# Optimization experiments

Measured on AMD Instinct MI355X. Metric: run time of the kernel, lower is better.

Reference implementation:

```python
import jax, jax.numpy as jnp
import numpy as np

N_CLASS = 32000
EMB = 512
HID = 1024
BATCH = 64
SEQ = 256


def setup_inputs() -> dict:
    key = jax.random.key(0)
    ks = jax.random.split(key, 24)
    X = jax.random.randint(ks[0], (BATCH, SEQ), 0, N_CLASS)
    C_emb = jax.random.normal(ks[1], (N_CLASS, EMB), dtype=jnp.float32) * 0.02
    d0 = HID + EMB   # layer-0 gate input dim (cat(h, x))
    d1 = HID + HID   # layer-1 gate input dim (cat(h, h_below))
    def w(k, din):
        return jax.random.normal(k, (din, HID), dtype=jnp.float32) * (1.0 / np.sqrt(din))
    inp = {
        'X': X, 'C_emb': C_emb,
        'W_i0': w(ks[2], d0), 'b_i0': jnp.ones((HID,), jnp.float32),
        'W_c0': w(ks[3], d0), 'b_c0': jnp.ones((HID,), jnp.float32),
        'W_f0': w(ks[4], d0), 'b_f0': jnp.ones((HID,), jnp.float32),
        'W_o0': w(ks[5], d0), 'b_o0': jnp.ones((HID,), jnp.float32),
        'W_i1': w(ks[6], d1), 'b_i1': jnp.ones((HID,), jnp.float32),
        'W_c1': w(ks[7], d1), 'b_c1': jnp.ones((HID,), jnp.float32),
        'W_f1': w(ks[8], d1), 'b_f1': jnp.ones((HID,), jnp.float32),
        'W_o1': w(ks[9], d1), 'b_o1': jnp.ones((HID,), jnp.float32),
        'W_out': jax.random.normal(ks[10], (HID, N_CLASS), jnp.float32) * (1.0 / np.sqrt(HID)),
        'b_out': jnp.ones((N_CLASS,), jnp.float32),
    }
    return inp


def _lstm_lm(X, C_emb, layers, W_out, b_out):
    B = X.shape[0]
    xs = jnp.transpose(C_emb[X], (1, 0, 2))  # (S, B, E)
    h0 = tuple(jnp.zeros((B, HID), xs.dtype) for _ in layers)
    c0 = tuple(jnp.zeros((B, HID), xs.dtype) for _ in layers)

    def step(carry, x_t):
        hs, cs = carry
        inp = x_t
        new_h, new_c = [], []
        for l, (Wi, bi, Wc, bc, Wf, bf, Wo, bo) in enumerate(layers):
            m = jnp.concatenate([hs[l], inp], axis=1)  # cat(h_state, input_below)
            i = jax.nn.sigmoid(m @ Wi + bi)
            g = jnp.tanh(m @ Wc + bc)
            f = jax.nn.sigmoid(m @ Wf + bf)
            c = f * cs[l] + i * g
            o = jax.nn.sigmoid(m @ Wo + bo)
            h = o * jnp.tanh(c)
            new_h.append(h)
            new_c.append(c)
            inp = h
        return (tuple(new_h), tuple(new_c)), None

    (hs, _), _ = jax.lax.scan(step, (h0, c0), xs)
    return hs[-1] @ W_out + b_out  # (B, n_class): logits from last timestep, top layer


def reference(X, C_emb, W_i0, b_i0, W_c0, b_c0, W_f0, b_f0, W_o0, b_o0,
              W_i1, b_i1, W_c1, b_c1, W_f1, b_f1, W_o1, b_o1, W_out, b_out):
    layers = [
        (W_i0, b_i0, W_c0, b_c0, W_f0, b_f0, W_o0, b_o0),
        (W_i1, b_i1, W_c1, b_c1, W_f1, b_f1, W_o1, b_o1),
    ]
    return _lstm_lm(X, C_emb, layers, W_out, b_out)
```

## Files before the change

### kernel.cpp

```cpp
#include <hip/hip_runtime.h>
#include <cstdint>
#include <cstddef>

#define NCLS 32000
#define EMBD 512
#define HIDD 1024
#define BATCH 64
#define SEQL 256
#define NWG 256
#define K0 1536
#define K1 2048
#define K0P (K0 + 2)
#define K1P (K1 + 2)
#define BH (BATCH * HIDD)
#define HBYTES (BH * 2)


typedef __attribute__((ext_vector_type(8))) short short8;
typedef __attribute__((ext_vector_type(4))) float float4v;
typedef unsigned long long ull;

#define WS_CTR   0
#define WS_H0G   2048
#define WS_H1G   (WS_H0G + 2*HBYTES)
#define WS_XEMB  (WS_H1G + 2*HBYTES)

#define SMEM_BYTES ((16*K0P + 16*K1P)*2 + (8192 + 32 + 512 + 8)*4)

__device__ __forceinline__ unsigned short f2bf(float f) {
  union { float f; uint32_t u; } x; x.f = f;
  uint32_t r = x.u + 0x7FFFu + ((x.u >> 16) & 1u);
  return (unsigned short)(r >> 16);
}

__device__ __forceinline__ float sigm(float x) {
  return 1.0f / (1.0f + __expf(-x));
}

__device__ __forceinline__ void gbar(unsigned* bar, unsigned* gen, unsigned* dead,
                                     unsigned target) {
  __syncthreads();
  if (threadIdx.x == 0) {
    unsigned prev = __hip_atomic_fetch_add(bar, 1u, __ATOMIC_RELAXED, __HIP_MEMORY_SCOPE_AGENT);
    if (prev == target * NWG - 1u) {
      __hip_atomic_store(gen, target, __ATOMIC_RELAXED, __HIP_MEMORY_SCOPE_AGENT);
    } else {
      unsigned spin = 0;
      while (__hip_atomic_load(gen, __ATOMIC_RELAXED, __HIP_MEMORY_SCOPE_AGENT) < target) {
        if (__hip_atomic_load(dead, __ATOMIC_RELAXED, __HIP_MEMORY_SCOPE_AGENT) != 0u) break;
        if (++spin > 2000000u) {
          __hip_atomic_store(dead, 1u, __ATOMIC_RELAXED, __HIP_MEMORY_SCOPE_AGENT);
          break;
        }
        __builtin_amdgcn_s_sleep(1);
      }
    }
  }
  __syncthreads();
}

__device__ __forceinline__ void hbar(unsigned* ctr, unsigned xcc, unsigned nloc,
                                     unsigned nxcd, unsigned tgt) {
  __syncthreads();
  if (threadIdx.x == 0) {
    unsigned* xctr = ctr + 64 + 16 * xcc;
    unsigned* xgen = ctr + 192 + 16 * xcc;
    unsigned* dead = ctr + 17;
    unsigned a = __hip_atomic_fetch_add(xctr, 1u, __ATOMIC_RELAXED, __HIP_MEMORY_SCOPE_AGENT);
    if (a == tgt * nloc - 1u) {
      asm volatile("buffer_inv sc1\n\ts_waitcnt vmcnt(0)" ::: "memory");
      unsigned g = __hip_atomic_fetch_add(ctr, 1u, __ATOMIC_RELAXED, __HIP_MEMORY_SCOPE_AGENT);
      if (g == tgt * nxcd - 1u) {
        __hip_atomic_store(ctr + 16, tgt, __ATOMIC_RELAXED, __HIP_MEMORY_SCOPE_AGENT);
      } else {
        unsigned spin = 0;
        while (__hip_atomic_load(ctr + 16, __ATOMIC_RELAXED, __HIP_MEMORY_SCOPE_AGENT) < tgt) {
          if ((++spin & 63u) == 0u) {
            if (__hip_atomic_load(dead, __ATOMIC_RELAXED, __HIP_MEMORY_SCOPE_AGENT) != 0u) break;
            if (spin > 4000000u) {
              __hip_atomic_store(dead, 1u, __ATOMIC_RELAXED, __HIP_MEMORY_SCOPE_AGENT);
              break;
            }
          }
        }
      }
      __hip_atomic_store(xgen, tgt, __ATOMIC_RELAXED, __HIP_MEMORY_SCOPE_AGENT);
    } else {
      unsigned spin = 0;
      while (__hip_atomic_load(xgen, __ATOMIC_RELAXED, __HIP_MEMORY_SCOPE_AGENT) < tgt) {
        if ((++spin & 63u) == 0u) {
          if (__hip_atomic_load(dead, __ATOMIC_RELAXED, __HIP_MEMORY_SCOPE_AGENT) != 0u) break;
          if (spin > 4000000u) {
            __hip_atomic_store(dead, 1u, __ATOMIC_RELAXED, __HIP_MEMORY_SCOPE_AGENT);
            break;
          }
        }
      }
    }
  }
  __syncthreads();
}

__global__ void init_bar_k(char* ws) {
  if (threadIdx.x < 320) ((unsigned*)(ws + WS_CTR))[threadIdx.x] = 0u;
}

__global__ void embed_k(const int* __restrict__ X, const float* __restrict__ Cemb,
                        char* __restrict__ ws) {
  uint32_t p = blockIdx.x * 256u + threadIdx.x;
  uint32_t t = p >> 14;
  uint32_t r = p & 16383u;
  uint32_t b = r >> 8;
  uint32_t e2 = r & 255u;
  int row = X[b * SEQL + t];
  const float2 v = *(const float2*)(Cemb + (size_t)row * EMBD + (size_t)e2 * 2);
  uint32_t lo = f2bf(v.x), hi = f2bf(v.y);
  uint32_t dw = t * 16384u + (e2 >> 4) * 1024u + b * 16u + (e2 & 15u);
  ((uint32_t*)(ws + WS_XEMB))[dw] = (hi << 16) | lo;
}

__global__ __launch_bounds__(512, 1)
void lstm_k(const float* __restrict__ Wi0, const float* __restrict__ Wc0,
            const float* __restrict__ Wf0, const float* __restrict__ Wo0,
            const float* __restrict__ Wi1, const float* __restrict__ Wc1,
            const float* __restrict__ Wf1, const float* __restrict__ Wo1,
            const float* __restrict__ bi0, const float* __restrict__ bc0,
            const float* __restrict__ bf0, const float* __restrict__ bo0,
            const float* __restrict__ bi1, const float* __restrict__ bc1,
            const float* __restrict__ bf1, const float* __restrict__ bo1,
            char* ws) {
  const int wg   = blockIdx.x;
  const int tid  = threadIdx.x;
  const int lane = tid & 63;
  const int wv   = tid >> 6;
  const int l15  = lane & 15;
  const int quad = lane >> 4;

  extern __shared__ char smem[];
  unsigned short* w0 = (unsigned short*)smem;
  unsigned short* w1 = w0 + 16 * K0P;
  float* red  = (float*)(w1 + 16 * K1P);
  float* bias = red + 8192;
  float* cst  = bias + 32;
  int*   meta = (int*)(cst + 512);

  unsigned short* h0buf = (unsigned short*)(ws + WS_H0G);
  unsigned short* h1buf = (unsigned short*)(ws + WS_H1G);
  const unsigned short* xemb = (const unsigned short*)(ws + WS_XEMB);
  unsigned* ctr = (unsigned*)(ws + WS_CTR);

  const unsigned xcc = __builtin_amdgcn_s_getreg((3u << 11) | 20u) & 7u;

  if (tid == 0)
    __hip_atomic_fetch_add(ctr + 32 + xcc, 1u, __ATOMIC_RELAXED, __HIP_MEMORY_SCOPE_AGENT);

  {
    const float* W0g[4] = {Wi0, Wc0, Wf0, Wo0};
    const float* W1g[4] = {Wi1, Wc1, Wf1, Wo1};
    int jl = tid & 3;
    int kr = tid >> 2;
    int jg = wg * 4 + jl;
    for (int g = 0; g < 4; ++g) {
      unsigned short* dst0 = w0 + (jl * 4 + g) * K0P;
      const float* s0 = W0g[g] + jg;
      for (int k = kr; k < K0; k += 128) dst0[k] = f2bf(s0[(size_t)k * HIDD]);
      unsigned short* dst1 = w1 + (jl * 4 + g) * K1P;
      const float* s1 = W1g[g] + jg;
      for (int k = kr; k < K1; k += 128) dst1[k] = f2bf(s1[(size_t)k * HIDD]);
    }
  }
  if (tid < 32) {
    const float* B0g[4] = {bi0, bc0, bf0, bo0};
    const float* B1g[4] = {bi1, bc1, bf1, bo1};
    int lay = tid >> 4, idx = tid & 15, jl = idx >> 2, g = idx & 3;
    bias[tid] = (lay ? B1g[g] : B0g[g])[wg * 4 + jl];
  }
  cst[tid] = 0.f;
  if (tid < 128) {
    unsigned short* base = (tid < 64) ? h0buf : h1buf;
    int b = tid & 63;
    __hip_atomic_store((ull*)(base + ((wg >> 3) << 11) + b * 32 + (wg & 7) * 4), 0ull,
                       __ATOMIC_RELAXED, __HIP_MEMORY_SCOPE_AGENT);
  }

  gbar(ctr + 48, ctr + 56, ctr + 17, 1u);

  if (tid == 0) {
    int nl = (int)__hip_atomic_load(ctr + 32 + xcc, __ATOMIC_RELAXED, __HIP_MEMORY_SCOPE_AGENT);
    int nx = 0;
    for (int x = 0; x < 8; ++x)
      nx += (__hip_atomic_load(ctr + 32 + x, __ATOMIC_RELAXED, __HIP_MEMORY_SCOPE_AGENT) != 0u);
    meta[0] = nl; meta[1] = nx;
  }
  __syncthreads();
  const unsigned nloc = (unsigned)meta[0], nxcd = (unsigned)meta[1];

  const int lofs = l15 * 32 + quad * 8;

  unsigned tgt = 0;
  for (int p = 0; p <= SEQL; ++p) {
    const int run0 = (p < SEQL);
    const int run1 = (p >= 1);
    if (wv < 4) {
      if (run0) {
        const unsigned short* hp = h0buf + (size_t)(p & 1) * BH;
        const unsigned short* xe = xemb + (size_t)p * BATCH * EMBD;
        float4v acc0 = {0.f,0.f,0.f,0.f}, acc1 = acc0, acc2 = acc0, acc3 = acc0;
        const int kbeg = wv * 384;
        #pragma unroll
        for (int bb = 0; bb < 2; ++bb) {
          short8 d[6][4];
          #pragma unroll
          for (int i = 0; i < 6; ++i) {
            int k0 = kbeg + (bb * 6 + i) * 32;
            const unsigned short* base =
              (k0 < HIDD) ? (hp + ((k0 >> 5) << 11)) : (xe + (((k0 - HIDD) >> 5) << 11));
            const unsigned short* ab = base + lofs;
            d[i][0] = *(const short8*)(ab);
            d[i][1] = *(const short8*)(ab + 512);
            d[i][2] = *(const short8*)(ab + 1024);
            d[i][3] = *(const short8*)(ab + 1536);
          }
          #pragma unroll
          for (int i = 0; i < 6; ++i) {
            int k0 = kbeg + (bb * 6 + i) * 32;
            short8 bfr = *(const short8*)(w0 + l15 * K0P + k0 + quad * 8);
            acc0 = __builtin_amdgcn_mfma_f32_16x16x32_bf16(d[i][0], bfr, acc0, 0, 0, 0);
            acc1 = __builtin_amdgcn_mfma_f32_16x16x32_bf16(d[i][1], bfr, acc1, 0, 0, 0);
            acc2 = __builtin_amdgcn_mfma_f32_16x16x32_bf16(d[i][2], bfr, acc2, 0, 0, 0);
            acc3 = __builtin_amdgcn_mfma_f32_16x16x32_bf16(d[i][3], bfr, acc3, 0, 0, 0);
          }
        }
        float* rw = red + wv * 1024 + quad * 64 + l15;
        #pragma unroll
        for (int r = 0; r < 4; ++r) {
          rw[r * 16]       = acc0[r];
          rw[256 + r * 16] = acc1[r];
          rw[512 + r * 16] = acc2[r];
          rw[768 + r * 16] = acc3[r];
        }
      }
    } else {
      if (run1) {
        const unsigned short* h1p = h1buf + (size_t)((p & 1) ^ 1) * BH;
        const unsigned short* h0c = h0buf + (size_t)(p & 1) * BH;
        float4v acc0 = {0.f,0.f,0.f,0.f}, acc1 = acc0, acc2 = acc0, acc3 = acc0;
        const int kbeg = (wv - 4) * 512;
        #pragma unroll
        for (int bb = 0; bb < 2; ++bb) {
          short8 d[8][4];
          #pragma unroll
          for (int i = 0; i < 8; ++i) {
            int k0 = kbeg + (bb * 8 + i) * 32;
            const unsigned short* base =
              (k0 < HIDD) ? (h1p + ((k0 >> 5) << 11)) : (h0c + (((k0 - HIDD) >> 5) << 11));
            const unsigned short* ab = base + lofs;
            d[i][0] = *(const short8*)(ab);
            d[i][1] = *(const short8*)(ab + 512);
            d[i][2] = *(const short8*)(ab + 1024);
            d[i][3] = *(const short8*)(ab + 1536);
          }
          #pragma unroll
          for (int i = 0; i < 8; ++i) {
            int k0 = kbeg + (bb * 8 + i) * 32;
            short8 bfr = *(const short8*)(w1 + l15 * K1P + k0 + quad * 8);
            acc0 = __builtin_amdgcn_mfma_f32_16x16x32_bf16(d[i][0], bfr, acc0, 0, 0, 0);
            acc1 = __builtin_amdgcn_mfma_f32_16x16x32_bf16(d[i][1], bfr, acc1, 0, 0, 0);
            acc2 = __builtin_amdgcn_mfma_f32_16x16x32_bf16(d[i][2], bfr, acc2, 0, 0, 0);
            acc3 = __builtin_amdgcn_mfma_f32_16x16x32_bf16(d[i][3], bfr, acc3, 0, 0, 0);
          }
        }
        float* rw = red + wv * 1024 + quad * 64 + l15;
        #pragma unroll
        for (int r = 0; r < 4; ++r) {
          rw[r * 16]       = acc0[r];
          rw[256 + r * 16] = acc1[r];
          rw[512 + r * 16] = acc2[r];
          rw[768 + r * 16] = acc3[r];
        }
      }
    }
    __syncthreads();
    if (tid < 256) {
      if (run0) {
        int b = tid >> 2, jl = tid & 3;
        const float* rr = red + b * 16 + jl * 4;
        float4v v = *(const float4v*)rr;
        v += *(const float4v*)(rr + 1024);
        v += *(const float4v*)(rr + 2048);
        v += *(const float4v*)(rr + 3072);
        float ig = sigm(v.x + bias[jl * 4 + 0]);
        float gg = tanhf(v.y + bias[jl * 4 + 1]);
        float fg = sigm(v.z + bias[jl * 4 + 2]);
        float og = sigm(v.w + bias[jl * 4 + 3]);
        float c = fg * cst[tid] + ig * gg;
        cst[tid] = c;
        unsigned x  = f2bf(og * tanhf(c));
        unsigned x1 = (unsigned)__shfl((int)x, lane + 1);
        unsigned x2 = (unsigned)__shfl((int)x, lane + 2);
        unsigned x3 = (unsigned)__shfl((int)x, lane + 3);
        if ((lane & 3) == 0) {
          ull val = (ull)(x | (x1 << 16)) | ((ull)(x2 | (x3 << 16)) << 32);
          unsigned short* dst = h0buf + (size_t)((p & 1) ^ 1) * BH
                              + ((wg >> 3) << 11) + b * 32 + (wg & 7) * 4;
          __hip_atomic_store((ull*)dst, val, __ATOMIC_RELAXED, __HIP_MEMORY_SCOPE_AGENT);
        }
      }
    } else {
      if (run1) {
        int t = tid - 256, b = t >> 2, jl = t & 3;
        const float* rr = red + 4096 + b * 16 + jl * 4;
        float4v v = *(const float4v*)rr;
        v += *(const float4v*)(rr + 1024);
        v += *(const float4v*)(rr + 2048);
        v += *(const float4v*)(rr + 3072);
        float ig = sigm(v.x + bias[16 + jl * 4 + 0]);
        float gg = tanhf(v.y + bias[16 + jl * 4 + 1]);
        float fg = sigm(v.z + bias[16 + jl * 4 + 2]);
        float og = sigm(v.w + bias[16 + jl * 4 + 3]);
        float c = fg * cst[tid] + ig * gg;
        cst[tid] = c;
        unsigned x  = f2bf(og * tanhf(c));
        unsigned x1 = (unsigned)__shfl((int)x, lane + 1);
        unsigned x2 = (unsigned)__shfl((int)x, lane + 2);
        unsigned x3 = (unsigned)__shfl((int)x, lane + 3);
        if ((lane & 3) == 0) {
          ull val = (ull)(x | (x1 << 16)) | ((ull)(x2 | (x3 << 16)) << 32);
          unsigned short* dst = h1buf + (size_t)(p & 1) * BH
                              + ((wg >> 3) << 11) + b * 32 + (wg & 7) * 4;
          __hip_atomic_store((ull*)dst, val, __ATOMIC_RELAXED, __HIP_MEMORY_SCOPE_AGENT);
        }
      }
    }
    if (p == SEQL) break;
    hbar(ctr, xcc, nloc, nxcd, ++tgt);
  }
}

__global__ __launch_bounds__(256, 1)
void out_gemm_k(const char* __restrict__ ws, const float* __restrict__ Wout,
                const float* __restrict__ bout, float* __restrict__ out) {
  const unsigned short* h1 = (const unsigned short*)(ws + WS_H1G);
  const int tid = threadIdx.x, lane = tid & 63, wv = tid >> 6;
  const int l15 = lane & 15, quad = lane >> 4;
  const int n0 = blockIdx.x * 128 + wv * 32;
  float4v acc[4][2];
  #pragma unroll
  for (int m = 0; m < 4; ++m)
    #pragma unroll
    for (int f = 0; f < 2; ++f) acc[m][f] = (float4v){0.f, 0.f, 0.f, 0.f};

  for (int k0 = 0; k0 < HIDD; k0 += 32) {
    const unsigned short* tb = h1 + ((k0 >> 5) << 11) + l15 * 32 + quad * 8;
    short8 a[4];
    #pragma unroll
    for (int m = 0; m < 4; ++m)
      a[m] = *(const short8*)(tb + m * 512);
    short8 bf[2];
    #pragma unroll
    for (int f = 0; f < 2; ++f) {
      int n = n0 + f * 16 + l15;
      #pragma unroll
      for (int j = 0; j < 8; ++j) {
        float w = Wout[(size_t)(k0 + quad * 8 + j) * NCLS + n];
        bf[f][j] = (short)f2bf(w);
      }
    }
    #pragma unroll
    for (int m = 0; m < 4; ++m)
      #pragma unroll
      for (int f = 0; f < 2; ++f)
        acc[m][f] = __builtin_amdgcn_mfma_f32_16x16x32_bf16(a[m], bf[f], acc[m][f], 0, 0, 0);
  }
  #pragma unroll
  for (int m = 0; m < 4; ++m)
    #pragma unroll
    for (int f = 0; f < 2; ++f) {
      int n = n0 + f * 16 + l15;
      float bb = bout[n];
      #pragma unroll
      for (int r = 0; r < 4; ++r) {
        int b = m * 16 + quad * 4 + r;
        out[(size_t)b * NCLS + n] = acc[m][f][r] + bb;
      }
    }
}

extern "C" void kernel_launch(void* const* d_in, const int* in_sizes, int n_in,
                              void* d_out, int out_size, void* d_ws, size_t ws_size,
                              hipStream_t stream) {
  const int*   X    = (const int*)d_in[0];
  const float* Cemb = (const float*)d_in[1];
  const float* Wi0  = (const float*)d_in[2];
  const float* bi0  = (const float*)d_in[3];
  const float* Wc0  = (const float*)d_in[4];
  const float* bc0  = (const float*)d_in[5];
  const float* Wf0  = (const float*)d_in[6];
  const float* bf0  = (const float*)d_in[7];
  const float* Wo0  = (const float*)d_in[8];
  const float* bo0  = (const float*)d_in[9];
  const float* Wi1  = (const float*)d_in[10];
  const float* bi1  = (const float*)d_in[11];
  const float* Wc1  = (const float*)d_in[12];
  const float* bc1  = (const float*)d_in[13];
  const float* Wf1  = (const float*)d_in[14];
  const float* bf1  = (const float*)d_in[15];
  const float* Wo1  = (const float*)d_in[16];
  const float* bo1  = (const float*)d_in[17];
  const float* Wout = (const float*)d_in[18];
  const float* bout = (const float*)d_in[19];
  float* out = (float*)d_out;
  char* ws = (char*)d_ws;

  hipFuncSetAttribute((const void*)lstm_k,
                      hipFuncAttributeMaxDynamicSharedMemorySize, SMEM_BYTES);

  init_bar_k<<<1, 512, 0, stream>>>(ws);
  embed_k<<<16384, 256, 0, stream>>>(X, Cemb, ws);
  lstm_k<<<NWG, 512, SMEM_BYTES, stream>>>(Wi0, Wc0, Wf0, Wo0, Wi1, Wc1, Wf1, Wo1,
                                           bi0, bc0, bf0, bo0, bi1, bc1, bf1, bo1, ws);
  out_gemm_k<<<250, 256, 0, stream>>>(ws, Wout, bout, out);
}
```

Baseline: 2.903 ms.

## Keep LSTM weights in registers and share layer-0 hidden state via LDS

Gate weights move from LDS into per-wave register fragments (bfr[16]), loaded once through a scratch LDS staging area. Layer-0 waves copy the h0 tiles they read into LDS so the layer-1 waves can reuse them instead of reloading from global memory. To allow this, the layer-1 gate GEMM is split into an h1 part, run alongside layer 0, and an h0 part, run after the layer-0 cell update. Bias and cell state move to registers. The cost is an extra __syncthreads per timestep and much higher register pressure.

Result: faster. 2.829 ms (-2.6%).

```diff
diff --git a/kernel.cpp b/kernel.cpp
--- a/kernel.cpp
+++ b/kernel.cpp
@@ -8,10 +8,6 @@
 #define BATCH 64
 #define SEQL 256
 #define NWG 256
-#define K0 1536
-#define K1 2048
-#define K0P (K0 + 2)
-#define K1P (K1 + 2)
 #define BH (BATCH * HIDD)
 #define HBYTES (BH * 2)
 
@@ -19,18 +15,21 @@
 typedef __attribute__((ext_vector_type(8))) short short8;
 typedef __attribute__((ext_vector_type(4))) float float4v;
 typedef unsigned long long ull;
+typedef unsigned short ushort;
 
 #define WS_CTR   0
 #define WS_H0G   2048
 #define WS_H1G   (WS_H0G + 2*HBYTES)
 #define WS_XEMB  (WS_H1G + 2*HBYTES)
 
-#define SMEM_BYTES ((16*K0P + 16*K1P)*2 + (8192 + 32 + 512 + 8)*4)
-
-__device__ __forceinline__ unsigned short f2bf(float f) {
+#define LDS_RED_OFF  126976
+#define LDS_META_OFF (126976 + 32768)
+#define SMEM_BYTES   (126976 + 32768 + 16)
+
+__device__ __forceinline__ ushort f2bf(float f) {
   union { float f; uint32_t u; } x; x.f = f;
   uint32_t r = x.u + 0x7FFFu + ((x.u >> 16) & 1u);
-  return (unsigned short)(r >> 16);
+  return (ushort)(r >> 16);
 }
 
 __device__ __forceinline__ float sigm(float x) {
@@ -137,16 +136,13 @@
   const int quad = lane >> 4;
 
   extern __shared__ char smem[];
-  unsigned short* w0 = (unsigned short*)smem;
-  unsigned short* w1 = w0 + 16 * K0P;
-  float* red  = (float*)(w1 + 16 * K1P);
-  float* bias = red + 8192;
-  float* cst  = bias + 32;
-  int*   meta = (int*)(cst + 512);
-
-  unsigned short* h0buf = (unsigned short*)(ws + WS_H0G);
-  unsigned short* h1buf = (unsigned short*)(ws + WS_H1G);
-  const unsigned short* xemb = (const unsigned short*)(ws + WS_XEMB);
+  ushort* h0st = (ushort*)smem;
+  float*  red  = (float*)(smem + LDS_RED_OFF);
+  int*    meta = (int*)(smem + LDS_META_OFF);
+
+  ushort* h0buf = (ushort*)(ws + WS_H0G);
+  ushort* h1buf = (ushort*)(ws + WS_H1G);
+  const ushort* xemb = (const ushort*)(ws + WS_XEMB);
   unsigned* ctr = (unsigned*)(ws + WS_CTR);
 
   const unsigned xcc = __builtin_amdgcn_s_getreg((3u << 11) | 20u) & 7u;
@@ -154,30 +150,55 @@
   if (tid == 0)
     __hip_atomic_fetch_add(ctr + 32 + xcc, 1u, __ATOMIC_RELAXED, __HIP_MEMORY_SCOPE_AGENT);
 
+  short8 bfr[16];
   {
-    const float* W0g[4] = {Wi0, Wc0, Wf0, Wo0};
-    const float* W1g[4] = {Wi1, Wc1, Wf1, Wo1};
-    int jl = tid & 3;
-    int kr = tid >> 2;
-    int jg = wg * 4 + jl;
-    for (int g = 0; g < 4; ++g) {
-      unsigned short* dst0 = w0 + (jl * 4 + g) * K0P;
-      const float* s0 = W0g[g] + jg;
-      for (int k = kr; k < K0; k += 128) dst0[k] = f2bf(s0[(size_t)k * HIDD]);
-      unsigned short* dst1 = w1 + (jl * 4 + g) * K1P;
-      const float* s1 = W1g[g] + jg;
-      for (int k = kr; k < K1; k += 128) dst1[k] = f2bf(s1[(size_t)k * HIDD]);
-    }
-  }
-  if (tid < 32) {
-    const float* B0g[4] = {bi0, bc0, bf0, bo0};
-    const float* B1g[4] = {bi1, bc1, bf1, bo1};
-    int lay = tid >> 4, idx = tid & 15, jl = idx >> 2, g = idx & 3;
-    bias[tid] = (lay ? B1g[g] : B0g[g])[wg * 4 + jl];
-  }
-  cst[tid] = 0.f;
+    ushort* scr = (ushort*)smem;
+    {
+      const float* W0g[4] = {Wi0, Wc0, Wf0, Wo0};
+      int jl = tid & 3, kr = tid >> 2, jg = wg * 4 + jl;
+      for (int g = 0; g < 4; ++g) {
+        ushort* dst = scr + (jl * 4 + g) * 1536;
+        const float* s = W0g[g] + jg;
+        for (int k = kr; k < 1536; k += 128) dst[k] = f2bf(s[(size_t)k * HIDD]);
+      }
+    }
+    __syncthreads();
+    if (wv < 4) {
+      #pragma unroll
+      for (int j = 0; j < 12; ++j)
+        bfr[j] = *(const short8*)(scr + l15 * 1536 + (12 * wv + j) * 32 + quad * 8);
+    }
+    __syncthreads();
+    {
+      const float* W1g[4] = {Wi1, Wc1, Wf1, Wo1};
+      int jl = tid & 3, kr = tid >> 2, jg = wg * 4 + jl;
+      for (int g = 0; g < 4; ++g) {
+        ushort* dst = scr + (jl * 4 + g) * 2048;
+        const float* s = W1g[g] + jg;
+        for (int k = kr; k < 2048; k += 128) dst[k] = f2bf(s[(size_t)k * HIDD]);
+      }
+    }
+    __syncthreads();
+    if (wv >= 4) {
+      #pragma unroll
+      for (int j = 0; j < 8; ++j)
+        bfr[j] = *(const short8*)(scr + l15 * 2048 + ((wv - 4) * 256 + j * 32) + quad * 8);
+      #pragma unroll
+      for (int j = 0; j < 8; ++j)
+        bfr[8 + j] = *(const short8*)(scr + l15 * 2048 + 1024 + ((wv - 4) * 256 + j * 32) + quad * 8);
+    }
+    __syncthreads();
+  }
+
+  float bs0 = 0.f, bs1 = 0.f, bs2 = 0.f, bs3 = 0.f, cstr = 0.f;
+  {
+    int jl = tid & 3, jg = wg * 4 + jl;
+    if (tid < 256) { bs0 = bi0[jg]; bs1 = bc0[jg]; bs2 = bf0[jg]; bs3 = bo0[jg]; }
+    else           { bs0 = bi1[jg]; bs1 = bc1[jg]; bs2 = bf1[jg]; bs3 = bo1[jg]; }
+  }
+
   if (tid < 128) {
-    unsigned short* base = (tid < 64) ? h0buf : h1buf;
+    ushort* base = (tid < 64) ? h0buf : h1buf;
     int b = tid & 63;
     __hip_atomic_store((ull*)(base + ((wg >> 3) << 11) + b * 32 + (wg & 7) * 4), 0ull,
                        __ATOMIC_RELAXED, __HIP_MEMORY_SCOPE_AGENT);
@@ -201,21 +222,20 @@
   for (int p = 0; p <= SEQL; ++p) {
     const int run0 = (p < SEQL);
     const int run1 = (p >= 1);
+    float4v acc0 = {0.f,0.f,0.f,0.f}, acc1 = acc0, acc2 = acc0, acc3 = acc0;
+
     if (wv < 4) {
       if (run0) {
-        const unsigned short* hp = h0buf + (size_t)(p & 1) * BH;
-        const unsigned short* xe = xemb + (size_t)p * BATCH * EMBD;
-        float4v acc0 = {0.f,0.f,0.f,0.f}, acc1 = acc0, acc2 = acc0, acc3 = acc0;
-        const int kbeg = wv * 384;
+        const ushort* hp = h0buf + (size_t)(p & 1) * BH;
+        const ushort* xe = xemb + (size_t)p * BATCH * EMBD;
         #pragma unroll
         for (int bb = 0; bb < 2; ++bb) {
           short8 d[6][4];
           #pragma unroll
           for (int i = 0; i < 6; ++i) {
-            int k0 = kbeg + (bb * 6 + i) * 32;
-            const unsigned short* base =
-              (k0 < HIDD) ? (hp + ((k0 >> 5) << 11)) : (xe + (((k0 - HIDD) >> 5) << 11));
-            const unsigned short* ab = base + lofs;
+            int kb = 12 * wv + bb * 6 + i;
+            const ushort* base = (kb < 32) ? (hp + kb * 2048) : (xe + (kb - 32) * 2048);
+            const ushort* ab = base + lofs;
             d[i][0] = *(const short8*)(ab);
             d[i][1] = *(const short8*)(ab + 512);
             d[i][2] = *(const short8*)(ab + 1024);
@@ -223,12 +243,19 @@
           }
           #pragma unroll
           for (int i = 0; i < 6; ++i) {
-            int k0 = kbeg + (bb * 6 + i) * 32;
-            short8 bfr = *(const short8*)(w0 + l15 * K0P + k0 + quad * 8);
-            acc0 = __builtin_amdgcn_mfma_f32_16x16x32_bf16(d[i][0], bfr, acc0, 0, 0, 0);
-            acc1 = __builtin_amdgcn_mfma_f32_16x16x32_bf16(d[i][1], bfr, acc1, 0, 0, 0);
-            acc2 = __builtin_amdgcn_mfma_f32_16x16x32_bf16(d[i][2], bfr, acc2, 0, 0, 0);
-            acc3 = __builtin_amdgcn_mfma_f32_16x16x32_bf16(d[i][3], bfr, acc3, 0, 0, 0);
+            int kb = 12 * wv + bb * 6 + i;
+            if (kb <= 30) {
+              ushort* sp = h0st + kb * 2048 + lofs;
+              *(short8*)(sp)        = d[i][0];
+              *(short8*)(sp + 512)  = d[i][1];
+              *(short8*)(sp + 1024) = d[i][2];
+              *(short8*)(sp + 1536) = d[i][3];
+            }
+            short8 w = bfr[bb * 6 + i];
+            acc0 = __builtin_amdgcn_mfma_f32_16x16x32_bf16(d[i][0], w, acc0, 0, 0, 0);
+            acc1 = __builtin_amdgcn_mfma_f32_16x16x32_bf16(d[i][1], w, acc1, 0, 0, 0);
+            acc2 = __builtin_amdgcn_mfma_f32_16x16x32_bf16(d[i][2], w, acc2, 0, 0, 0);
+            acc3 = __builtin_amdgcn_mfma_f32_16x16x32_bf16(d[i][3], w, acc3, 0, 0, 0);
           }
         }
         float* rw = red + wv * 1024 + quad * 64 + l15;
@@ -242,94 +269,121 @@
       }
     } else {
       if (run1) {
-        const unsigned short* h1p = h1buf + (size_t)((p & 1) ^ 1) * BH;
-        const unsigned short* h0c = h0buf + (size_t)(p & 1) * BH;
-        float4v acc0 = {0.f,0.f,0.f,0.f}, acc1 = acc0, acc2 = acc0, acc3 = acc0;
-        const int kbeg = (wv - 4) * 512;
+        const ushort* h1p = h1buf + (size_t)((p & 1) ^ 1) * BH;
         #pragma unroll
         for (int bb = 0; bb < 2; ++bb) {
-          short8 d[8][4];
+          short8 d[4][4];
           #pragma unroll
-          for (int i = 0; i < 8; ++i) {
-            int k0 = kbeg + (bb * 8 + i) * 32;
-            const unsigned short* base =
-              (k0 < HIDD) ? (h1p + ((k0 >> 5) << 11)) : (h0c + (((k0 - HIDD) >> 5) << 11));
-            const unsigned short* ab = base + lofs;
+          for (int i = 0; i < 4; ++i) {
+            int kb = (wv - 4) * 8 + bb * 4 + i;
+            const ushort* ab = h1p + kb * 2048 + lofs;
             d[i][0] = *(const short8*)(ab);
             d[i][1] = *(const short8*)(ab + 512);
             d[i][2] = *(const short8*)(ab + 1024);
             d[i][3] = *(const short8*)(ab + 1536);
           }
           #pragma unroll
-          for (int i = 0; i < 8; ++i) {
-            int k0 = kbeg + (bb * 8 + i) * 32;
-            short8 bfr = *(const short8*)(w1 + l15 * K1P + k0 + quad * 8);
-            acc0 = __builtin_amdgcn_mfma_f32_16x16x32_bf16(d[i][0], bfr, acc0, 0, 0, 0);
-            acc1 = __builtin_amdgcn_mfma_f32_16x16x32_bf16(d[i][1], bfr, acc1, 0, 0, 0);
-            acc2 = __builtin_amdgcn_mfma_f32_16x16x32_bf16(d[i][2], bfr, acc2, 0, 0, 0);
-            acc3 = __builtin_amdgcn_mfma_f32_16x16x32_bf16(d[i][3], bfr, acc3, 0, 0, 0);
-          }
-        }
-        float* rw = red + wv * 1024 + quad * 64 + l15;
+          for (int i = 0; i < 4; ++i) {
+            short8 w = bfr[bb * 4 + i];
+            acc0 = __builtin_amdgcn_mfma_f32_16x16x32_bf16(d[i][0], w, acc0, 0, 0, 0);
+            acc1 = __builtin_amdgcn_mfma_f32_16x16x32_bf16(d[i][1], w, acc1, 0, 0, 0);
+            acc2 = __builtin_amdgcn_mfma_f32_16x16x32_bf16(d[i][2], w, acc2, 0, 0, 0);
+            acc3 = __builtin_amdgcn_mfma_f32_16x16x32_bf16(d[i][3], w, acc3, 0, 0, 0);
+          }
+        }
+      }
+    }
+    __syncthreads();
+
+    if (run0 && tid < 256) {
+      int b = tid >> 2;
+      const float* rr = red + b * 16 + (tid & 3) * 4;
+      float4v v = *(const float4v*)rr;
+      v += *(const float4v*)(rr + 1024);
+      v += *(const float4v*)(rr + 2048);
+      v += *(const float4v*)(rr + 3072);
+      float ig = sigm(v.x + bs0);
+      float gg = tanhf(v.y + bs1);
+      float fg = sigm(v.z + bs2);
+      float og = sigm(v.w + bs3);
+      float c = fg * cstr + ig * gg;
+      cstr = c;
+      unsigned x  = f2bf(og * tanhf(c));
+      unsigned x1 = (unsigned)__shfl((int)x, lane + 1);
+      unsigned x2 = (unsigned)__shfl((int)x, lane + 2);
+      unsigned x3 = (unsigned)__shfl((int)x, lane + 3);
+      if ((lane & 3) == 0) {
+        ull val = (ull)(x | (x1 << 16)) | ((ull)(x2 | (x3 << 16)) << 32);
+        ushort* dst = h0buf + (size_t)((p & 1) ^ 1) * BH
+                    + ((wg >> 3) << 11) + b * 32 + (wg & 7) * 4;
+        __hip_atomic_store((ull*)dst, val, __ATOMIC_RELAXED, __HIP_MEMORY_SCOPE_AGENT);
+      }
+    }
+    if (run1 && wv >= 4) {
+      const ushort* h0c = h0buf + (size_t)(p & 1) * BH;
+      const bool useLds = (p < SEQL);
+      #pragma unroll
+      for (int bb = 0; bb < 2; ++bb) {
+        short8 d[4][4];
         #pragma unroll
-        for (int r = 0; r < 4; ++r) {
-          rw[r * 16]       = acc0[r];
-          rw[256 + r * 16] = acc1[r];
-          rw[512 + r * 16] = acc2[r];
-          rw[768 + r * 16] = acc3[r];
-        }
-      }
-    }
-    __syncthreads();
-    if (tid < 256) {
-      if (run0) {
-        int b = tid >> 2, jl = tid & 3;
-        const float* rr = red + b * 16 + jl * 4;
-        float4v v = *(const float4v*)rr;
-        v += *(const float4v*)(rr + 1024);
-        v += *(const float4v*)(rr + 2048);
-        v += *(const float4v*)(rr + 3072);
-        float ig = sigm(v.x + bias[jl * 4 + 0]);
-        float gg = tanhf(v.y + bias[jl * 4 + 1]);
-        float fg = sigm(v.z + bias[jl * 4 + 2]);
-        float og = sigm(v.w + bias[jl * 4 + 3]);
-        float c = fg * cst[tid] + ig * gg;
-        cst[tid] = c;
-        unsigned x  = f2bf(og * tanhf(c));
-        unsigned x1 = (unsigned)__shfl((int)x, lane + 1);
-        unsigned x2 = (unsigned)__shfl((int)x, lane + 2);
-        unsigned x3 = (unsigned)__shfl((int)x, lane + 3);
-        if ((lane & 3) == 0) {
-          ull val = (ull)(x | (x1 << 16)) | ((ull)(x2 | (x3 << 16)) << 32);
-          unsigned short* dst = h0buf + (size_t)((p & 1) ^ 1) * BH
-                              + ((wg >> 3) << 11) + b * 32 + (wg & 7) * 4;
-          __hip_atomic_store((ull*)dst, val, __ATOMIC_RELAXED, __HIP_MEMORY_SCOPE_AGENT);
-        }
-      }
-    } else {
-      if (run1) {
-        int t = tid - 256, b = t >> 2, jl = t & 3;
-        const float* rr = red + 4096 + b * 16 + jl * 4;
-        float4v v = *(const float4v*)rr;
-        v += *(const float4v*)(rr + 1024);
-        v += *(const float4v*)(rr + 2048);
-        v += *(const float4v*)(rr + 3072);
-        float ig = sigm(v.x + bias[16 + jl * 4 + 0]);
-        float gg = tanhf(v.y + bias[16 + jl * 4 + 1]);
-        float fg = sigm(v.z + bias[16 + jl * 4 + 2]);
-        float og = sigm(v.w + bias[16 + jl * 4 + 3]);
-        float c = fg * cst[tid] + ig * gg;
-        cst[tid] = c;
-        unsigned x  = f2bf(og * tanhf(c));
-        unsigned x1 = (unsigned)__shfl((int)x, lane + 1);
-        unsigned x2 = (unsigned)__shfl((int)x, lane + 2);
-        unsigned x3 = (unsigned)__shfl((int)x, lane + 3);
-        if ((lane & 3) == 0) {
-          ull val = (ull)(x | (x1 << 16)) | ((ull)(x2 | (x3 << 16)) << 32);
-          unsigned short* dst = h1buf + (size_t)(p & 1) * BH
-                              + ((wg >> 3) << 11) + b * 32 + (wg & 7) * 4;
-          __hip_atomic_store((ull*)dst, val, __ATOMIC_RELAXED, __HIP_MEMORY_SCOPE_AGENT);
-        }
+        for (int i = 0; i < 4; ++i) {
+          int kb = (wv - 4) * 8 + bb * 4 + i;
+          if (useLds && kb <= 30) {
+            const ushort* sp = h0st + kb * 2048 + lofs;
+            d[i][0] = *(const short8*)(sp);
+            d[i][1] = *(const short8*)(sp + 512);
+            d[i][2] = *(const short8*)(sp + 1024);
+            d[i][3] = *(const short8*)(sp + 1536);
+          } else {
+            const ushort* ab = h0c + kb * 2048 + lofs;
+            d[i][0] = *(const short8*)(ab);
+            d[i][1] = *(const short8*)(ab + 512);
+            d[i][2] = *(const short8*)(ab + 1024);
+            d[i][3] = *(const short8*)(ab + 1536);
+          }
+        }
+        #pragma unroll
+        for (int i = 0; i < 4; ++i) {
+          short8 w = bfr[8 + bb * 4 + i];
+          acc0 = __builtin_amdgcn_mfma_f32_16x16x32_bf16(d[i][0], w, acc0, 0, 0, 0);
+          acc1 = __builtin_amdgcn_mfma_f32_16x16x32_bf16(d[i][1], w, acc1, 0, 0, 0);
+          acc2 = __builtin_amdgcn_mfma_f32_16x16x32_bf16(d[i][2], w, acc2, 0, 0, 0);
+          acc3 = __builtin_amdgcn_mfma_f32_16x16x32_bf16(d[i][3], w, acc3, 0, 0, 0);
+        }
+      }
+      float* rw = red + wv * 1024 + quad * 64 + l15;
+      #pragma unroll
+      for (int r = 0; r < 4; ++r) {
+        rw[r * 16]       = acc0[r];
+        rw[256 + r * 16] = acc1[r];
+        rw[512 + r * 16] = acc2[r];
+        rw[768 + r * 16] = acc3[r];
+      }
+    }
+    __syncthreads();
+
+    if (run1 && tid >= 256) {
+      int t = tid - 256, b = t >> 2;
+      const float* rr = red + 4096 + b * 16 + (t & 3) * 4;
+      float4v v = *(const float4v*)rr;
+      v += *(const float4v*)(rr + 1024);
+      v += *(const float4v*)(rr + 2048);
+      v += *(const float4v*)(rr + 3072);
+      float ig = sigm(v.x + bs0);
+      float gg = tanhf(v.y + bs1);
+      float fg = sigm(v.z + bs2);
+      float og = sigm(v.w + bs3);
+      float c = fg * cstr + ig * gg;
+      cstr = c;
+      unsigned x  = f2bf(og * tanhf(c));
+      unsigned x1 = (unsigned)__shfl((int)x, lane + 1);
+      unsigned x2 = (unsigned)__shfl((int)x, lane + 2);
+      unsigned x3 = (unsigned)__shfl((int)x, lane + 3);
+      if ((lane & 3) == 0) {
+        ull val = (ull)(x | (x1 << 16)) | ((ull)(x2 | (x3 << 16)) << 32);
+        ushort* dst = h1buf + (size_t)(p & 1) * BH
+                    + ((wg >> 3) << 11) + b * 32 + (wg & 7) * 4;
+        __hip_atomic_store((ull*)dst, val, __ATOMIC_RELAXED, __HIP_MEMORY_SCOPE_AGENT);
       }
     }
     if (p == SEQL) break;
@@ -340,7 +394,7 @@
 __global__ __launch_bounds__(256, 1)
 void out_gemm_k(const char* __restrict__ ws, const float* __restrict__ Wout,
                 const float* __restrict__ bout, float* __restrict__ out) {
-  const unsigned short* h1 = (const unsigned short*)(ws + WS_H1G);
+  const ushort* h1 = (const ushort*)(ws + WS_H1G);
   const int tid = threadIdx.x, lane = tid & 63, wv = tid >> 6;
   const int l15 = lane & 15, quad = lane >> 4;
   const int n0 = blockIdx.x * 128 + wv * 32;
@@ -351,7 +405,7 @@
     for (int f = 0; f < 2; ++f) acc[m][f] = (float4v){0.f, 0.f, 0.f, 0.f};
 
   for (int k0 = 0; k0 < HIDD; k0 += 32) {
-    const unsigned short* tb = h1 + ((k0 >> 5) << 11) + l15 * 32 + quad * 8;
+    const ushort* tb = h1 + ((k0 >> 5) << 11) + l15 * 32 + quad * 8;
     short8 a[4];
     #pragma unroll
     for (int m = 0; m < 4; ++m)
```
